# Performance work log

Measured on AMD Instinct MI355X. Metric: run time of the kernel, lower is better.

## Reference

```python
import jax, jax.numpy as jnp
import numpy as np

N_NODES = 50000
N_EDGES = 1600000
IN_C, HID_C, OUT_C = 64, 64, 7


def setup_inputs() -> dict:
    key = jax.random.key(0)
    ks = jax.random.split(key, 8)
    x = jax.random.normal(ks[0], (N_NODES, IN_C), dtype=jnp.float32)
    edge_index = jax.random.randint(ks[1], (2, N_EDGES), 0, N_NODES, dtype=jnp.int64)
    s_in = 1.0 / np.sqrt(IN_C)
    s_hid = 1.0 / np.sqrt(HID_C)
    W1 = jax.random.normal(ks[2], (HID_C, IN_C), dtype=jnp.float32) * s_in
    b1 = jnp.zeros((HID_C,), dtype=jnp.float32)
    W2 = jax.random.normal(ks[3], (HID_C, HID_C), dtype=jnp.float32) * s_hid
    b2 = jnp.zeros((HID_C,), dtype=jnp.float32)
    W3 = jax.random.normal(ks[4], (OUT_C, HID_C), dtype=jnp.float32) * s_hid
    b3 = jnp.zeros((OUT_C,), dtype=jnp.float32)
    return {"x": x, "edge_index": edge_index, "W1": W1, "b1": b1,
            "W2": W2, "b2": b2, "W3": W3, "b3": b3}


def _gcn_conv(x, src, dst, W, b):
    # GCNConv(normalize=False): lin -> sum-aggregate over incoming edges -> +bias
    h = x @ W.T                                   # [N, out]
    msg = h[src]                                  # gather source features [E, out]
    agg = jax.ops.segment_sum(msg, dst, num_segments=N_NODES)  # scatter-add
    return agg + b


def reference(x, edge_index, W1, b1, W2, b2, W3, b3):
    src, dst = edge_index[0], edge_index[1]
    h = jax.nn.relu(_gcn_conv(x, src, dst, W1, b1))   # dropout is identity in eval
    h = jax.nn.relu(_gcn_conv(h, src, dst, W2, b2))
    h = _gcn_conv(h, src, dst, W3, b3)
    return jax.nn.log_softmax(h, axis=-1)
```

## Files before the change

kernel.cpp:

```cpp
#include <hip/hip_runtime.h>
#include <math.h>

#define N_NODES 50000
#define N_EDGES 1600000
#define C 64
#define OUTC 7

#define NB 196
#define BCAP 10240
#define CHUNK 8192

typedef __attribute__((ext_vector_type(8))) short bf16x8;
typedef __attribute__((ext_vector_type(4))) float f32x4;

__device__ __forceinline__ unsigned int pk_bf16(float a, float b) {
    unsigned int ua = __float_as_uint(a);
    ua = (ua + 0x7FFFu + ((ua >> 16) & 1u)) >> 16;
    unsigned int ub = __float_as_uint(b);
    ub = (ub + 0x7FFFu + ((ub >> 16) & 1u)) >> 16;
    return ua | (ub << 16);
}

union U4B8 { uint4 u; bf16x8 s; };

__global__ __launch_bounds__(256) void bin_kernel(const int* __restrict__ src,
                                                  const int* __restrict__ dst,
                                                  unsigned int* __restrict__ buckets,
                                                  int* __restrict__ gcursor) {
    __shared__ unsigned int staged[CHUNK];
    __shared__ int hist[NB], scanb[NB], cur[NB], baseb[NB];
    const int tid = threadIdx.x;
    const int base = blockIdx.x * CHUNK;
    int n = N_EDGES - base; if (n > CHUNK) n = CHUNK;

    for (int b = tid; b < NB; b += 256) { hist[b] = 0; cur[b] = 0; }
    __syncthreads();

    const int4* src4 = (const int4*)(src + base);
    const int4* dst4 = (const int4*)(dst + base);
    unsigned int v[32];
    int nv = n >> 2;
#pragma unroll
    for (int k = 0; k < 8; ++k) {
        int i4 = k * 256 + tid;
        if (i4 < nv) {
            int4 s4 = src4[i4];
            int4 d4 = dst4[i4];
            unsigned int d0 = (unsigned int)d4.x, d1 = (unsigned int)d4.y;
            unsigned int d2 = (unsigned int)d4.z, d3 = (unsigned int)d4.w;
            v[k * 4 + 0] = (d0 << 16) | (unsigned int)s4.x;
            v[k * 4 + 1] = (d1 << 16) | (unsigned int)s4.y;
            v[k * 4 + 2] = (d2 << 16) | (unsigned int)s4.z;
            v[k * 4 + 3] = (d3 << 16) | (unsigned int)s4.w;
            atomicAdd(&hist[d0 >> 8], 1);
            atomicAdd(&hist[d1 >> 8], 1);
            atomicAdd(&hist[d2 >> 8], 1);
            atomicAdd(&hist[d3 >> 8], 1);
        }
    }
    __syncthreads();
    if (tid == 0) {
        int run = 0;
        for (int b = 0; b < NB; ++b) { scanb[b] = run; run += hist[b]; }
    }
    __syncthreads();
#pragma unroll
    for (int k = 0; k < 8; ++k) {
        int i4 = k * 256 + tid;
        if (i4 < nv) {
#pragma unroll
            for (int q = 0; q < 4; ++q) {
                unsigned int w = v[k * 4 + q];
                int b = w >> 24;
                int p = scanb[b] + atomicAdd(&cur[b], 1);
                staged[p] = w;
            }
        }
    }
    __syncthreads();
    if (tid < NB) baseb[tid] = atomicAdd(&gcursor[tid], hist[tid]);
    __syncthreads();
    for (int i = tid; i < n; i += 256) {
        unsigned int w = staged[i];
        int b = w >> 24;
        buckets[(size_t)b * BCAP + baseb[b] + (i - scanb[b])] = w;
    }
}

__global__ __launch_bounds__(256) void build_csr(const unsigned int* __restrict__ buckets,
                                                 const int* __restrict__ gcursor,
                                                 unsigned int* __restrict__ csr,
                                                 int* __restrict__ off) {
    __shared__ int hist[256], part[256], offx[256], cur[256];
    __shared__ int gl[NB];
    __shared__ int s_cnt, s_base;
    const int tid = threadIdx.x;
    const int b = blockIdx.x;

    hist[tid] = 0;
    cur[tid] = 0;
    if (tid < NB) gl[tid] = gcursor[tid];
    __syncthreads();
    if (tid == 0) {
        int bs = 0;
        for (int i = 0; i < b; ++i) bs += gl[i];
        s_base = bs;
        s_cnt = gl[b];
    }
    __syncthreads();
    const int cnt = s_cnt;
    const int gbase = s_base;
    const unsigned int* bk = buckets + (size_t)b * BCAP;

    for (int i = tid; i < cnt; i += 256) {
        atomicAdd(&hist[(bk[i] >> 16) & 255], 1);
    }
    __syncthreads();
    part[tid] = hist[tid];
    __syncthreads();
    for (int d = 1; d < 256; d <<= 1) {
        int t = (tid >= d) ? part[tid - d] : 0;
        __syncthreads();
        part[tid] += t;
        __syncthreads();
    }
    offx[tid] = (tid == 0) ? 0 : part[tid - 1];
    __syncthreads();
    int node = b * 256 + tid;
    if (node < N_NODES) off[node] = gbase + offx[tid];
    if (b == NB - 1 && tid == 0) off[N_NODES] = gbase + cnt;
    for (int i = tid; i < cnt; i += 256) {
        unsigned int w = bk[i];
        int dl = (w >> 16) & 255;
        int p = offx[dl] + atomicAdd(&cur[dl], 1);
        csr[gbase + p] = w & 0xFFFFu;
    }
}


__global__ __launch_bounds__(256) void pack_w(const float* __restrict__ W,
                                              unsigned int* __restrict__ Wb) {
    int idx = blockIdx.x * 256 + threadIdx.x;
    if (idx >= 64 * 32) return;
    const float2* w2 = (const float2*)W;
    float2 v = w2[idx];
    Wb[idx] = pk_bf16(v.x, v.y);
}


__global__ __launch_bounds__(256) void linear64_mfma_x(const float* __restrict__ x,
                                                       const unsigned int* __restrict__ Wb,
                                                       unsigned int* __restrict__ out) {
    const int wave = threadIdx.x >> 6;
    const int lane = threadIdx.x & 63;
    const int quad = lane >> 4;
    const int l16  = lane & 15;
    const int rbase = blockIdx.x * 64 + wave * 16;
    if (rbase >= N_NODES) return;

    U4B8 bfrag[4][2];
#pragma unroll
    for (int ct = 0; ct < 4; ++ct)
#pragma unroll
        for (int kt = 0; kt < 2; ++kt)
            bfrag[ct][kt].u = *(const uint4*)(Wb + (ct * 16 + l16) * 32 + kt * 16 + quad * 4);

    U4B8 afrag[2];
#pragma unroll
    for (int kt = 0; kt < 2; ++kt) {
        const float4* xp = (const float4*)(x + (size_t)(rbase + l16) * 64 + kt * 32 + quad * 8);
        float4 f0 = xp[0];
        float4 f1 = xp[1];
        afrag[kt].u.x = pk_bf16(f0.x, f0.y);
        afrag[kt].u.y = pk_bf16(f0.z, f0.w);
        afrag[kt].u.z = pk_bf16(f1.x, f1.y);
        afrag[kt].u.w = pk_bf16(f1.z, f1.w);
    }

    f32x4 acc[4];
#pragma unroll
    for (int ct = 0; ct < 4; ++ct) {
        f32x4 z = {0.f, 0.f, 0.f, 0.f};
        z = __builtin_amdgcn_mfma_f32_16x16x32_bf16(afrag[0].s, bfrag[ct][0].s, z, 0, 0, 0);
        z = __builtin_amdgcn_mfma_f32_16x16x32_bf16(afrag[1].s, bfrag[ct][1].s, z, 0, 0, 0);
        acc[ct] = z;
    }

    const int colp = l16 >> 1;
    const bool even = (l16 & 1) == 0;
#pragma unroll
    for (int ct = 0; ct < 4; ++ct) {
#pragma unroll
        for (int i = 0; i < 4; ++i) {
            float v = acc[ct][i];
            float p = __shfl_xor(v, 1, 64);
            if (even) {
                int row = rbase + quad * 4 + i;
                out[(size_t)row * 32 + ct * 8 + colp] = pk_bf16(v, p);
            }
        }
    }
}

__global__ __launch_bounds__(256) void linear64_mfma(const unsigned int* __restrict__ in,
                                                     const unsigned int* __restrict__ Wb,
                                                     unsigned int* __restrict__ out) {
    const int wave = threadIdx.x >> 6;
    const int lane = threadIdx.x & 63;
    const int quad = lane >> 4;
    const int l16  = lane & 15;
    const int rbase = blockIdx.x * 64 + wave * 16;
    if (rbase >= N_NODES) return;

    U4B8 bfrag[4][2];
#pragma unroll
    for (int ct = 0; ct < 4; ++ct)
#pragma unroll
        for (int kt = 0; kt < 2; ++kt)
            bfrag[ct][kt].u = *(const uint4*)(Wb + (ct * 16 + l16) * 32 + kt * 16 + quad * 4);

    U4B8 afrag[2];
#pragma unroll
    for (int kt = 0; kt < 2; ++kt)
        afrag[kt].u = *(const uint4*)(in + (size_t)(rbase + l16) * 32 + kt * 16 + quad * 4);

    f32x4 acc[4];
#pragma unroll
    for (int ct = 0; ct < 4; ++ct) {
        f32x4 z = {0.f, 0.f, 0.f, 0.f};
        z = __builtin_amdgcn_mfma_f32_16x16x32_bf16(afrag[0].s, bfrag[ct][0].s, z, 0, 0, 0);
        z = __builtin_amdgcn_mfma_f32_16x16x32_bf16(afrag[1].s, bfrag[ct][1].s, z, 0, 0, 0);
        acc[ct] = z;
    }

    const int colp = l16 >> 1;
    const bool even = (l16 & 1) == 0;
#pragma unroll
    for (int ct = 0; ct < 4; ++ct) {
#pragma unroll
        for (int i = 0; i < 4; ++i) {
            float v = acc[ct][i];
            float p = __shfl_xor(v, 1, 64);
            if (even) {
                int row = rbase + quad * 4 + i;
                out[(size_t)row * 32 + ct * 8 + colp] = pk_bf16(v, p);
            }
        }
    }
}

__global__ __launch_bounds__(128) void linear7_h(const unsigned int* __restrict__ hb,
                                                 const float* __restrict__ W,
                                                 unsigned int* __restrict__ out) {
    int r = blockIdx.x * 128 + threadIdx.x;
    if (r >= N_NODES) return;
    float xf[64];
    const uint4* hp = (const uint4*)(hb + (size_t)r * 32);
#pragma unroll
    for (int j = 0; j < 8; ++j) {
        uint4 u = hp[j];
        xf[j * 8 + 0] = __uint_as_float(u.x << 16);
        xf[j * 8 + 1] = __uint_as_float(u.x & 0xFFFF0000u);
        xf[j * 8 + 2] = __uint_as_float(u.y << 16);
        xf[j * 8 + 3] = __uint_as_float(u.y & 0xFFFF0000u);
        xf[j * 8 + 4] = __uint_as_float(u.z << 16);
        xf[j * 8 + 5] = __uint_as_float(u.z & 0xFFFF0000u);
        xf[j * 8 + 6] = __uint_as_float(u.w << 16);
        xf[j * 8 + 7] = __uint_as_float(u.w & 0xFFFF0000u);
    }

    float acc[7] = {0.f, 0.f, 0.f, 0.f, 0.f, 0.f, 0.f};
#pragma unroll
    for (int k = 0; k < 64; ++k) {
        float xv = xf[k];
#pragma unroll
        for (int j = 0; j < 7; ++j)
            acc[j] += xv * W[j * 64 + k];
    }
    uint4 w;
    w.x = pk_bf16(acc[0], acc[1]);
    w.y = pk_bf16(acc[2], acc[3]);
    w.z = pk_bf16(acc[4], acc[5]);
    w.w = pk_bf16(acc[6], 0.f);
    ((uint4*)(out + (size_t)r * 4))[0] = w;
}

__global__ __launch_bounds__(256) void gather64b(const int* __restrict__ off,
                                                 const unsigned int* __restrict__ csr_src,
                                                 const unsigned int* __restrict__ tb,
                                                 const float* __restrict__ b,
                                                 unsigned int* __restrict__ hb) {
    int node = blockIdx.x * 4 + (threadIdx.x >> 6);
    if (node >= N_NODES) return;
    const int lane = threadIdx.x & 63;
    const int slot = lane >> 3;
    const int ch8  = lane & 7;
    int e0 = off[node], e1 = off[node + 1];
    const uint4* t4 = (const uint4*)tb;
    float s[8] = {0.f, 0.f, 0.f, 0.f, 0.f, 0.f, 0.f, 0.f};
    for (int e = e0; e < e1; e += 32) {
        int i0 = e + slot;
        int i1 = e + 8 + slot;
        int i2 = e + 16 + slot;
        int i3 = e + 24 + slot;
        bool p0 = i0 < e1, p1 = i1 < e1, p2 = i2 < e1, p3 = i3 < e1;
        unsigned int a0 = csr_src[p0 ? i0 : e];
        unsigned int a1 = csr_src[p1 ? i1 : e];
        unsigned int a2 = csr_src[p2 ? i2 : e];
        unsigned int a3 = csr_src[p3 ? i3 : e];
        uint4 v0 = t4[(size_t)a0 * 8 + ch8];
        uint4 v1 = t4[(size_t)a1 * 8 + ch8];
        uint4 v2 = t4[(size_t)a2 * 8 + ch8];
        uint4 v3 = t4[(size_t)a3 * 8 + ch8];
        if (p0) {
            s[0] += __uint_as_float(v0.x << 16);
            s[1] += __uint_as_float(v0.x & 0xFFFF0000u);
            s[2] += __uint_as_float(v0.y << 16);
            s[3] += __uint_as_float(v0.y & 0xFFFF0000u);
            s[4] += __uint_as_float(v0.z << 16);
            s[5] += __uint_as_float(v0.z & 0xFFFF0000u);
            s[6] += __uint_as_float(v0.w << 16);
            s[7] += __uint_as_float(v0.w & 0xFFFF0000u);
        }
        if (p1) {
            s[0] += __uint_as_float(v1.x << 16);
            s[1] += __uint_as_float(v1.x & 0xFFFF0000u);
            s[2] += __uint_as_float(v1.y << 16);
            s[3] += __uint_as_float(v1.y & 0xFFFF0000u);
            s[4] += __uint_as_float(v1.z << 16);
            s[5] += __uint_as_float(v1.z & 0xFFFF0000u);
            s[6] += __uint_as_float(v1.w << 16);
            s[7] += __uint_as_float(v1.w & 0xFFFF0000u);
        }
        if (p2) {
            s[0] += __uint_as_float(v2.x << 16);
            s[1] += __uint_as_float(v2.x & 0xFFFF0000u);
            s[2] += __uint_as_float(v2.y << 16);
            s[3] += __uint_as_float(v2.y & 0xFFFF0000u);
            s[4] += __uint_as_float(v2.z << 16);
            s[5] += __uint_as_float(v2.z & 0xFFFF0000u);
            s[6] += __uint_as_float(v2.w << 16);
            s[7] += __uint_as_float(v2.w & 0xFFFF0000u);
        }
        if (p3) {
            s[0] += __uint_as_float(v3.x << 16);
            s[1] += __uint_as_float(v3.x & 0xFFFF0000u);
            s[2] += __uint_as_float(v3.y << 16);
            s[3] += __uint_as_float(v3.y & 0xFFFF0000u);
            s[4] += __uint_as_float(v3.z << 16);
            s[5] += __uint_as_float(v3.z & 0xFFFF0000u);
            s[6] += __uint_as_float(v3.w << 16);
            s[7] += __uint_as_float(v3.w & 0xFFFF0000u);
        }
    }
#pragma unroll
    for (int d = 8; d <= 32; d <<= 1) {
#pragma unroll
        for (int j = 0; j < 8; ++j) s[j] += __shfl_xor(s[j], d, 64);
    }
    if (lane < 8) {
        const float4 b0 = ((const float4*)b)[ch8 * 2];
        const float4 b1 = ((const float4*)b)[ch8 * 2 + 1];
        float r0 = fmaxf(s[0] + b0.x, 0.f);
        float r1 = fmaxf(s[1] + b0.y, 0.f);
        float r2 = fmaxf(s[2] + b0.z, 0.f);
        float r3 = fmaxf(s[3] + b0.w, 0.f);
        float r4 = fmaxf(s[4] + b1.x, 0.f);
        float r5 = fmaxf(s[5] + b1.y, 0.f);
        float r6 = fmaxf(s[6] + b1.z, 0.f);
        float r7 = fmaxf(s[7] + b1.w, 0.f);
        uint4 w;
        w.x = pk_bf16(r0, r1);
        w.y = pk_bf16(r2, r3);
        w.z = pk_bf16(r4, r5);
        w.w = pk_bf16(r6, r7);
        ((uint4*)(hb + (size_t)node * 32))[ch8] = w;
    }
}

__global__ __launch_bounds__(256) void gather7_lsm(const int* __restrict__ off,
                                                   const unsigned int* __restrict__ csr_src,
                                                   const unsigned int* __restrict__ t3,
                                                   const float* __restrict__ b,
                                                   float* __restrict__ out) {
    int node = blockIdx.x * 4 + (threadIdx.x >> 6);
    if (node >= N_NODES) return;
    const int lane = threadIdx.x & 63;
    const int slot = lane >> 1;
    const int h    = lane & 1;
    int e0 = off[node], e1 = off[node + 1];
    const uint2* t2 = (const uint2*)t3;
    float sx = 0.f, sy = 0.f, sz = 0.f, sw = 0.f;
    for (int e = e0 + slot; e < e1; e += 32) {
        unsigned int s = csr_src[e];
        uint2 v = t2[(size_t)s * 2 + h];
        sx += __uint_as_float(v.x << 16);
        sy += __uint_as_float(v.x & 0xFFFF0000u);
        sz += __uint_as_float(v.y << 16);
        sw += __uint_as_float(v.y & 0xFFFF0000u);
    }
#pragma unroll
    for (int d = 2; d <= 32; d <<= 1) {
        sx += __shfl_xor(sx, d, 64); sy += __shfl_xor(sy, d, 64);
        sz += __shfl_xor(sz, d, 64); sw += __shfl_xor(sw, d, 64);
    }
    float z0 = sx + b[h * 4 + 0];
    float z1 = sy + b[h * 4 + 1];
    float z2 = sz + b[h * 4 + 2];
    float z3 = (h == 0) ? (sw + b[3]) : -1e30f;
    float m = fmaxf(fmaxf(z0, z1), fmaxf(z2, z3));
    m = fmaxf(m, __shfl_xor(m, 1, 64));
    float ex = __expf(z0 - m) + __expf(z1 - m) + __expf(z2 - m) + __expf(z3 - m);
    ex += __shfl_xor(ex, 1, 64);
    float l = m + __logf(ex);
    if (lane < 2) {
        float* o = out + (size_t)node * 7 + h * 4;
        o[0] = z0 - l; o[1] = z1 - l; o[2] = z2 - l;
        if (h == 0) o[3] = z3 - l;
    }
}

extern "C" void kernel_launch(void* const* d_in, const int* in_sizes, int n_in,
                              void* d_out, int out_size, void* d_ws, size_t ws_size,
                              hipStream_t stream) {
    const float* x  = (const float*)d_in[0];
    const int*   ei = (const int*)d_in[1];
    const float* W1 = (const float*)d_in[2];
    const float* b1 = (const float*)d_in[3];
    const float* W2 = (const float*)d_in[4];
    const float* b2 = (const float*)d_in[5];
    const float* W3 = (const float*)d_in[6];
    const float* b3 = (const float*)d_in[7];
    float* out = (float*)d_out;

    const int* src = ei;
    const int* dst = ei + N_EDGES;

    float* A = (float*)d_ws;
    float* B = A + (size_t)N_NODES * C;
    unsigned int* csr = (unsigned int*)(B + (size_t)N_NODES * C);
    int* off     = (int*)(csr + N_EDGES);
    int* gcursor = off + N_NODES + 8;
    unsigned int* Wb1 = (unsigned int*)(gcursor + 256);
    unsigned int* Wb2 = Wb1 + 2048;
    unsigned int* buckets = (unsigned int*)A;
    unsigned int* Abf     = (unsigned int*)A;
    unsigned int* Hbf     = (unsigned int*)B;

    const int mfmagrid = (N_NODES + 63) / 64;
    const int l7grid   = (N_NODES + 127) / 128;
    const int ngrid    = (N_NODES + 3) / 4;

    pack_w<<<8, 256, 0, stream>>>(W1, Wb1);
    pack_w<<<8, 256, 0, stream>>>(W2, Wb2);

    (void)hipMemsetAsync(gcursor, 0, NB * sizeof(int), stream);
    bin_kernel<<<(N_EDGES + CHUNK - 1) / CHUNK, 256, 0, stream>>>(src, dst, buckets, gcursor);
    build_csr<<<NB, 256, 0, stream>>>(buckets, gcursor, csr, off);

    linear64_mfma_x<<<mfmagrid, 256, 0, stream>>>(x, Wb1, Abf);
    gather64b<<<ngrid, 256, 0, stream>>>(off, csr, Abf, b1, Hbf);

    linear64_mfma<<<mfmagrid, 256, 0, stream>>>(Hbf, Wb2, Abf);
    gather64b<<<ngrid, 256, 0, stream>>>(off, csr, Abf, b2, Hbf);

    linear7_h<<<l7grid, 128, 0, stream>>>(Hbf, W3, Abf);
    gather7_lsm<<<ngrid, 256, 0, stream>>>(off, csr, Abf, b3, out);
}
```

Before: 221.9 us.

## Fuse layer-3 linear into second gather, merge prep kernels, use nontemporal accesses

The second gather kernel now applies bias and ReLU, then multiplies by W3 in-register and writes the 7-wide bf16 projection directly. This removes the separate linear7_h pass and the round trip of the 64-wide hidden tensor through memory. The two weight-packing launches and the memset are merged into one prep kernel to cut launch overhead. CSR index loads and hidden-state stores become nontemporal to reduce cache pollution, at the cost of some extra shuffles per node in the fused kernel.

```diff
diff --git a/kernel.cpp b/kernel.cpp
--- a/kernel.cpp
+++ b/kernel.cpp
@@ -12,6 +12,7 @@
 
 typedef __attribute__((ext_vector_type(8))) short bf16x8;
 typedef __attribute__((ext_vector_type(4))) float f32x4;
+typedef __attribute__((ext_vector_type(4))) unsigned int u32x4;
 
 __device__ __forceinline__ unsigned int pk_bf16(float a, float b) {
     unsigned int ua = __float_as_uint(a);
@@ -22,6 +23,26 @@
 }
 
 union U4B8 { uint4 u; bf16x8 s; };
+
+__global__ __launch_bounds__(256) void prep(const float* __restrict__ W1,
+                                            const float* __restrict__ W2,
+                                            unsigned int* __restrict__ Wb1,
+                                            unsigned int* __restrict__ Wb2,
+                                            int* __restrict__ gcursor) {
+    const int b = blockIdx.x;
+    const int tid = threadIdx.x;
+    if (b < 8) {
+        int idx = b * 256 + tid;
+        float2 v = ((const float2*)W1)[idx];
+        Wb1[idx] = pk_bf16(v.x, v.y);
+    } else if (b < 16) {
+        int idx = (b - 8) * 256 + tid;
+        float2 v = ((const float2*)W2)[idx];
+        Wb2[idx] = pk_bf16(v.x, v.y);
+    } else {
+        if (tid < NB) gcursor[tid] = 0;
+    }
+}
 
 __global__ __launch_bounds__(256) void bin_kernel(const int* __restrict__ src,
                                                   const int* __restrict__ dst,
@@ -138,16 +159,6 @@
 }
 
 
-__global__ __launch_bounds__(256) void pack_w(const float* __restrict__ W,
-                                              unsigned int* __restrict__ Wb) {
-    int idx = blockIdx.x * 256 + threadIdx.x;
-    if (idx >= 64 * 32) return;
-    const float2* w2 = (const float2*)W;
-    float2 v = w2[idx];
-    Wb[idx] = pk_bf16(v.x, v.y);
-}
-
-
 __global__ __launch_bounds__(256) void linear64_mfma_x(const float* __restrict__ x,
                                                        const unsigned int* __restrict__ Wb,
                                                        unsigned int* __restrict__ out) {
@@ -247,42 +258,6 @@
             }
         }
     }
-}
-
-__global__ __launch_bounds__(128) void linear7_h(const unsigned int* __restrict__ hb,
-                                                 const float* __restrict__ W,
-                                                 unsigned int* __restrict__ out) {
-    int r = blockIdx.x * 128 + threadIdx.x;
-    if (r >= N_NODES) return;
-    float xf[64];
-    const uint4* hp = (const uint4*)(hb + (size_t)r * 32);
-#pragma unroll
-    for (int j = 0; j < 8; ++j) {
-        uint4 u = hp[j];
-        xf[j * 8 + 0] = __uint_as_float(u.x << 16);
-        xf[j * 8 + 1] = __uint_as_float(u.x & 0xFFFF0000u);
-        xf[j * 8 + 2] = __uint_as_float(u.y << 16);
-        xf[j * 8 + 3] = __uint_as_float(u.y & 0xFFFF0000u);
-        xf[j * 8 + 4] = __uint_as_float(u.z << 16);
-        xf[j * 8 + 5] = __uint_as_float(u.z & 0xFFFF0000u);
-        xf[j * 8 + 6] = __uint_as_float(u.w << 16);
-        xf[j * 8 + 7] = __uint_as_float(u.w & 0xFFFF0000u);
-    }
-
-    float acc[7] = {0.f, 0.f, 0.f, 0.f, 0.f, 0.f, 0.f};
-#pragma unroll
-    for (int k = 0; k < 64; ++k) {
-        float xv = xf[k];
-#pragma unroll
-        for (int j = 0; j < 7; ++j)
-            acc[j] += xv * W[j * 64 + k];
-    }
-    uint4 w;
-    w.x = pk_bf16(acc[0], acc[1]);
-    w.y = pk_bf16(acc[2], acc[3]);
-    w.z = pk_bf16(acc[4], acc[5]);
-    w.w = pk_bf16(acc[6], 0.f);
-    ((uint4*)(out + (size_t)r * 4))[0] = w;
 }
 
 __global__ __launch_bounds__(256) void gather64b(const int* __restrict__ off,
@@ -304,10 +279,10 @@
         int i2 = e + 16 + slot;
         int i3 = e + 24 + slot;
         bool p0 = i0 < e1, p1 = i1 < e1, p2 = i2 < e1, p3 = i3 < e1;
-        unsigned int a0 = csr_src[p0 ? i0 : e];
-        unsigned int a1 = csr_src[p1 ? i1 : e];
-        unsigned int a2 = csr_src[p2 ? i2 : e];
-        unsigned int a3 = csr_src[p3 ? i3 : e];
+        unsigned int a0 = __builtin_nontemporal_load(csr_src + (p0 ? i0 : e));
+        unsigned int a1 = __builtin_nontemporal_load(csr_src + (p1 ? i1 : e));
+        unsigned int a2 = __builtin_nontemporal_load(csr_src + (p2 ? i2 : e));
+        unsigned int a3 = __builtin_nontemporal_load(csr_src + (p3 ? i3 : e));
         uint4 v0 = t4[(size_t)a0 * 8 + ch8];
         uint4 v1 = t4[(size_t)a1 * 8 + ch8];
         uint4 v2 = t4[(size_t)a2 * 8 + ch8];
@@ -369,12 +344,119 @@
         float r5 = fmaxf(s[5] + b1.y, 0.f);
         float r6 = fmaxf(s[6] + b1.z, 0.f);
         float r7 = fmaxf(s[7] + b1.w, 0.f);
-        uint4 w;
+        u32x4 w;
         w.x = pk_bf16(r0, r1);
         w.y = pk_bf16(r2, r3);
         w.z = pk_bf16(r4, r5);
         w.w = pk_bf16(r6, r7);
-        ((uint4*)(hb + (size_t)node * 32))[ch8] = w;
+        __builtin_nontemporal_store(w, (u32x4*)(hb + (size_t)node * 32) + ch8);
+    }
+}
+
+__global__ __launch_bounds__(256) void gather64b_w3(const int* __restrict__ off,
+                                                    const unsigned int* __restrict__ csr_src,
+                                                    const unsigned int* __restrict__ tb,
+                                                    const float* __restrict__ b,
+                                                    const float* __restrict__ W3,
+                                                    unsigned int* __restrict__ t3) {
+    int node = blockIdx.x * 4 + (threadIdx.x >> 6);
+    if (node >= N_NODES) return;
+    const int lane = threadIdx.x & 63;
+    const int slot = lane >> 3;
+    const int ch8  = lane & 7;
+    int e0 = off[node], e1 = off[node + 1];
+    const uint4* t4 = (const uint4*)tb;
+    float s[8] = {0.f, 0.f, 0.f, 0.f, 0.f, 0.f, 0.f, 0.f};
+    for (int e = e0; e < e1; e += 32) {
+        int i0 = e + slot;
+        int i1 = e + 8 + slot;
+        int i2 = e + 16 + slot;
+        int i3 = e + 24 + slot;
+        bool p0 = i0 < e1, p1 = i1 < e1, p2 = i2 < e1, p3 = i3 < e1;
+        unsigned int a0 = __builtin_nontemporal_load(csr_src + (p0 ? i0 : e));
+        unsigned int a1 = __builtin_nontemporal_load(csr_src + (p1 ? i1 : e));
+        unsigned int a2 = __builtin_nontemporal_load(csr_src + (p2 ? i2 : e));
+        unsigned int a3 = __builtin_nontemporal_load(csr_src + (p3 ? i3 : e));
+        uint4 v0 = t4[(size_t)a0 * 8 + ch8];
+        uint4 v1 = t4[(size_t)a1 * 8 + ch8];
+        uint4 v2 = t4[(size_t)a2 * 8 + ch8];
+        uint4 v3 = t4[(size_t)a3 * 8 + ch8];
+        if (p0) {
+            s[0] += __uint_as_float(v0.x << 16);
+            s[1] += __uint_as_float(v0.x & 0xFFFF0000u);
+            s[2] += __uint_as_float(v0.y << 16);
+            s[3] += __uint_as_float(v0.y & 0xFFFF0000u);
+            s[4] += __uint_as_float(v0.z << 16);
+            s[5] += __uint_as_float(v0.z & 0xFFFF0000u);
+            s[6] += __uint_as_float(v0.w << 16);
+            s[7] += __uint_as_float(v0.w & 0xFFFF0000u);
+        }
+        if (p1) {
+            s[0] += __uint_as_float(v1.x << 16);
+            s[1] += __uint_as_float(v1.x & 0xFFFF0000u);
+            s[2] += __uint_as_float(v1.y << 16);
+            s[3] += __uint_as_float(v1.y & 0xFFFF0000u);
+            s[4] += __uint_as_float(v1.z << 16);
+            s[5] += __uint_as_float(v1.z & 0xFFFF0000u);
+            s[6] += __uint_as_float(v1.w << 16);
+            s[7] += __uint_as_float(v1.w & 0xFFFF0000u);
+        }
+        if (p2) {
+            s[0] += __uint_as_float(v2.x << 16);
+            s[1] += __uint_as_float(v2.x & 0xFFFF0000u);
+            s[2] += __uint_as_float(v2.y << 16);
+            s[3] += __uint_as_float(v2.y & 0xFFFF0000u);
+            s[4] += __uint_as_float(v2.z << 16);
+            s[5] += __uint_as_float(v2.z & 0xFFFF0000u);
+            s[6] += __uint_as_float(v2.w << 16);
+            s[7] += __uint_as_float(v2.w & 0xFFFF0000u);
+        }
+        if (p3) {
+            s[0] += __uint_as_float(v3.x << 16);
+            s[1] += __uint_as_float(v3.x & 0xFFFF0000u);
+            s[2] += __uint_as_float(v3.y << 16);
+            s[3] += __uint_as_float(v3.y & 0xFFFF0000u);
+            s[4] += __uint_as_float(v3.z << 16);
+            s[5] += __uint_as_float(v3.z & 0xFFFF0000u);
+            s[6] += __uint_as_float(v3.w << 16);
+            s[7] += __uint_as_float(v3.w & 0xFFFF0000u);
+        }
+    }
+#pragma unroll
+    for (int d = 8; d <= 32; d <<= 1) {
+#pragma unroll
+        for (int j = 0; j < 8; ++j) s[j] += __shfl_xor(s[j], d, 64);
+    }
+    const float4 b0 = ((const float4*)b)[ch8 * 2];
+    const float4 b1 = ((const float4*)b)[ch8 * 2 + 1];
+    float r[8];
+    r[0] = fmaxf(s[0] + b0.x, 0.f);
+    r[1] = fmaxf(s[1] + b0.y, 0.f);
+    r[2] = fmaxf(s[2] + b0.z, 0.f);
+    r[3] = fmaxf(s[3] + b0.w, 0.f);
+    r[4] = fmaxf(s[4] + b1.x, 0.f);
+    r[5] = fmaxf(s[5] + b1.y, 0.f);
+    r[6] = fmaxf(s[6] + b1.z, 0.f);
+    r[7] = fmaxf(s[7] + b1.w, 0.f);
+    float p[7];
+#pragma unroll
+    for (int j = 0; j < 7; ++j) {
+        const float4 wa = *(const float4*)(W3 + j * 64 + ch8 * 8);
+        const float4 wb = *(const float4*)(W3 + j * 64 + ch8 * 8 + 4);
+        float t = r[0] * wa.x + r[1] * wa.y + r[2] * wa.z + r[3] * wa.w
+                + r[4] * wb.x + r[5] * wb.y + r[6] * wb.z + r[7] * wb.w;
+        t += __shfl_xor(t, 1, 64);
+        t += __shfl_xor(t, 2, 64);
+        t += __shfl_xor(t, 4, 64);
+        p[j] = t;
+    }
+    if (lane == 0) {
+        u32x4 w;
+        w.x = pk_bf16(p[0], p[1]);
+        w.y = pk_bf16(p[2], p[3]);
+        w.z = pk_bf16(p[4], p[5]);
+        w.w = pk_bf16(p[6], 0.f);
+        __builtin_nontemporal_store(w, (u32x4*)(t3 + (size_t)node * 4));
     }
 }
 
@@ -392,7 +474,7 @@
     const uint2* t2 = (const uint2*)t3;
     float sx = 0.f, sy = 0.f, sz = 0.f, sw = 0.f;
     for (int e = e0 + slot; e < e1; e += 32) {
-        unsigned int s = csr_src[e];
+        unsigned int s = __builtin_nontemporal_load(csr_src + e);
         uint2 v = t2[(size_t)s * 2 + h];
         sx += __uint_as_float(v.x << 16);
         sy += __uint_as_float(v.x & 0xFFFF0000u);
@@ -446,15 +528,13 @@
     unsigned int* buckets = (unsigned int*)A;
     unsigned int* Abf     = (unsigned int*)A;
     unsigned int* Hbf     = (unsigned int*)B;
+    unsigned int* T3      = (unsigned int*)B;
 
     const int mfmagrid = (N_NODES + 63) / 64;
-    const int l7grid   = (N_NODES + 127) / 128;
     const int ngrid    = (N_NODES + 3) / 4;
 
-    pack_w<<<8, 256, 0, stream>>>(W1, Wb1);
-    pack_w<<<8, 256, 0, stream>>>(W2, Wb2);
-
-    (void)hipMemsetAsync(gcursor, 0, NB * sizeof(int), stream);
+    prep<<<17, 256, 0, stream>>>(W1, W2, Wb1, Wb2, gcursor);
+
     bin_kernel<<<(N_EDGES + CHUNK - 1) / CHUNK, 256, 0, stream>>>(src, dst, buckets, gcursor);
     build_csr<<<NB, 256, 0, stream>>>(buckets, gcursor, csr, off);
 
@@ -462,8 +542,8 @@
     gather64b<<<ngrid, 256, 0, stream>>>(off, csr, Abf, b1, Hbf);
 
     linear64_mfma<<<mfmagrid, 256, 0, stream>>>(Hbf, Wb2, Abf);
-    gather64b<<<ngrid, 256, 0, stream>>>(off, csr, Abf, b2, Hbf);
-
-    linear7_h<<<l7grid, 128, 0, stream>>>(Hbf, W3, Abf);
-    gather7_lsm<<<ngrid, 256, 0, stream>>>(off, csr, Abf, b3, out);
-}
+
+    gather64b_w3<<<ngrid, 256, 0, stream>>>(off, csr, Abf, b2, W3, T3);
+
+    gather7_lsm<<<ngrid, 256, 0, stream>>>(off, csr, T3, b3, out);
+}
```

Result: slower. 243.4 us (+9.7%).
